# Performance work log

Measured on AMD Instinct MI355X. Metric: run time of the kernel, lower is better.

Reference implementation:

```python
import jax, jax.numpy as jnp
import numpy as np
import math

HIDDEN = 8
HEADS = 2
HEAD_DIM = HIDDEN // HEADS  # 4
MAX_SEQ = 102
B, S = 4096, 102


def _rotary_cache(seq_len, head_dim):
    # Matches _create_rotary_embeddings: dim = head_dim//2, inv_freq over arange(0, dim, 2)
    pos = jnp.arange(seq_len, dtype=jnp.float32)
    dim = head_dim // 2
    inv_freq = 1.0 / (10000.0 ** (jnp.arange(0, dim, 2, dtype=jnp.float32) / dim))
    sinusoid = pos[:, None] * inv_freq[None, :]           # [seq, dim//2] -> [102, 1]
    return jnp.stack([jnp.sin(sinusoid), jnp.cos(sinusoid)], axis=0)  # [2, seq, 1]


def _apply_rotary(x, cos, sin):
    # x: [B, H, S, hd]; cos/sin: [2, S, 1] (faithful to the source's buggy unpack,
    # which broadcasts the stacked sin/cos pair across the H==2 head dim)
    x2 = jnp.stack([-x[..., 1::2], x[..., ::2]], axis=-1).reshape(x.shape)
    return x * cos + x2 * sin


def setup_inputs() -> dict:
    key = jax.random.key(0)
    kq, kk, kv, k1, k2, k3, k4 = jax.random.split(key, 7)
    scale = 1.0 / math.sqrt(HIDDEN)
    return {
        "query": jax.random.normal(kq, (B, S, HIDDEN), dtype=jnp.float32),
        "key": jax.random.normal(kk, (B, S, HIDDEN), dtype=jnp.float32),
        "value": jax.random.normal(kv, (B, S, HIDDEN), dtype=jnp.float32),
        "wq": jax.random.normal(k1, (HIDDEN, HIDDEN), dtype=jnp.float32) * scale,
        "wk": jax.random.normal(k2, (HIDDEN, HIDDEN), dtype=jnp.float32) * scale,
        "wv": jax.random.normal(k3, (HIDDEN, HIDDEN), dtype=jnp.float32) * scale,
        "wo": jax.random.normal(k4, (HIDDEN, HIDDEN), dtype=jnp.float32) * scale,
    }


def reference(query, key, value, wq, wk, wv, wo):
    b, sq, _ = query.shape
    sk = key.shape[1]
    # nn.Linear (no bias): y = x @ W^T
    q = query @ wq.T
    k = key @ wk.T
    v = value @ wv.T
    # b n (h d) -> b h n d
    def split_heads(t, s):
        return t.reshape(b, s, HEADS, HEAD_DIM).transpose(0, 2, 1, 3)
    q = split_heads(q, sq)
    k = split_heads(k, sk)
    v = split_heads(v, sk)
    cache = _rotary_cache(MAX_SEQ, HEAD_DIM)
    sin_t = cache[:, :sq]  # [2, sq, 1] (named 'sin' in source, holds stacked sin/cos)
    cos_t = cache[:, :sk]  # [2, sk, 1]
    q = _apply_rotary(q, cos_t, sin_t)
    k = _apply_rotary(k, cos_t, sin_t)
    scale = 1.0 / math.sqrt(HEAD_DIM)
    # chunk_size = min(sk, 1024) = sk -> single chunk == full softmax attention
    scores = jnp.einsum('bhqd,bhkd->bhqk', q, k) * scale  # [B, H, Sq, Sk]
    attn = jax.nn.softmax(scores, axis=-1)
    out = jnp.einsum('bhqk,bhkd->bhqd', attn, v)
    # b h n d -> b n (h d)
    out = out.transpose(0, 2, 1, 3).reshape(b, sq, HIDDEN)
    return out @ wo.T
```

## Files before the change

### kernel.cpp

```cpp
#include <hip/hip_runtime.h>

#define NB 4096
#define SS 102
#define SSP 104
#define HID 8
#define NH 2
#define HD 4

typedef float v2f __attribute__((ext_vector_type(2)));

__global__ __launch_bounds__(256) void mha_fused_kernel(
    const float* __restrict__ query, const float* __restrict__ key,
    const float* __restrict__ value, const float* __restrict__ wq,
    const float* __restrict__ wk, const float* __restrict__ wv,
    const float* __restrict__ wo, float* __restrict__ out)
{
    __shared__ float sRaw[3 * SS * HID];
    __shared__ float sQ[NH * SSP * HD];
    __shared__ float sK[NH * SS * HD];
    __shared__ float sV[NH * SS * HD];
    __shared__ float sW[4 * 64];
    __shared__ float sRot[2 * SS];

    const int t = threadIdx.x;
    const int b = blockIdx.x;

    float4 rq, rk, rv;
    if (t < 204) {
        const float4* q4 = (const float4*)(query + (size_t)b * (SS * HID));
        const float4* k4 = (const float4*)(key   + (size_t)b * (SS * HID));
        const float4* v4 = (const float4*)(value + (size_t)b * (SS * HID));
        rq = q4[t]; rk = k4[t]; rv = v4[t];
    }
    float wreg;
    {
        const float* wsrc = (t < 64) ? wq : (t < 128) ? wk : (t < 192) ? wv : wo;
        wreg = wsrc[t & 63];
    }

    if (t < SS)                    sRot[t] = __sinf((float)t);
    else if (t >= 128 && t < 230)  sRot[SS + (t - 128)] = __cosf((float)(t - 128));

    if (t >= 230 && t < 246) {
        const int z = t - 230;
        const int h = z >> 3, r = SS + ((z >> 2) & 1), d = z & 3;
        sQ[h * SSP * HD + r * HD + d] = 0.f;
    }

    sW[t] = wreg;
    if (t < 204) {
        float4* sRaw4 = (float4*)sRaw;
        sRaw4[t]       = rq;
        sRaw4[204 + t] = rk;
        sRaw4[408 + t] = rv;
    }
    __syncthreads();

    for (int p = t; p < 816; p += 256) {
        const int tensor = (p >= 408) ? 1 : 0;
        const int pp = tensor ? (p - 408) : p;
        const int s  = pp >> 2;
        const int pr = pp & 3;
        const int i0 = pr * 2, i1 = i0 + 1;
        const float4* raw4 = (const float4*)(sRaw + tensor * (SS * HID) + s * HID);
        const float4 ra = raw4[0], rb = raw4[1];
        const float4* w0 = (const float4*)(sW + tensor * 64 + i0 * 8);
        const float4 wa = w0[0], wb = w0[1], wc = w0[2], wd = w0[3];
        float x0 = ra.x * wa.x + ra.y * wa.y + ra.z * wa.z + ra.w * wa.w
                 + rb.x * wb.x + rb.y * wb.y + rb.z * wb.z + rb.w * wb.w;
        float x1 = ra.x * wc.x + ra.y * wc.y + ra.z * wc.z + ra.w * wc.w
                 + rb.x * wd.x + rb.y * wd.y + rb.z * wd.z + rb.w * wd.w;
        const int h = pr >> 1;
        float wr = sRot[h * SS + s];
        if (tensor == 0) wr *= 0.72134752044448170368f;
        const float r0 = (x0 - x1) * wr;
        const float r1 = (x1 + x0) * wr;
        const int d0 = i0 & 3;
        float* dst = (tensor == 0)
            ? (sQ + h * SSP * HD + s * HD + d0)
            : (sK + h * SS * HD + s * HD + d0);
        dst[0] = r0;
        dst[1] = r1;
    }
    for (int e = t; e < 816; e += 256) {
        const int s = e >> 3, i = e & 7;
        const float4* raw4 = (const float4*)(sRaw + 2 * (SS * HID) + s * HID);
        const float4 ra = raw4[0], rb = raw4[1];
        const float4* w0 = (const float4*)(sW + 2 * 64 + i * 8);
        const float4 wa = w0[0], wb = w0[1];
        const float x = ra.x * wa.x + ra.y * wa.y + ra.z * wa.z + ra.w * wa.w
                      + rb.x * wb.x + rb.y * wb.y + rb.z * wb.z + rb.w * wb.w;
        const int h = i >> 2, d = i & 3;
        sV[h * SS * HD + s * HD + d] = x;
    }
    __syncthreads();

    const int wv_  = t >> 6, lane = t & 63;
    const int h    = wv_ >> 1;
    const int kh   = wv_ & 1;
    const bool act = lane < 52;
    v2f acc0 = {0.f, 0.f}, acc1 = {0.f, 0.f}, acc2 = {0.f, 0.f}, acc3 = {0.f, 0.f};
    v2f l = {0.f, 0.f};
    if (act) {
        const float* qb = sQ + h * SSP * HD + (2 * lane) * HD;
        const float4 qa = ((const float4*)qb)[0];
        const float4 qc = ((const float4*)qb)[1];
        const v2f q0 = {qa.x, qc.x}, q1 = {qa.y, qc.y},
                  q2 = {qa.z, qc.z}, q3 = {qa.w, qc.w};
        const float4* K4 = (const float4*)(sK + h * SS * HD) + kh * 51;
        const float4* V4 = (const float4*)(sV + h * SS * HD) + kh * 51;
        float4 kk = K4[0], vvv = V4[0];
#pragma unroll 2
        for (int k = 1; k < 51; ++k) {
            const float4 nk = K4[k], nv = V4[k];
            v2f s = q0 * kk.x + q1 * kk.y + q2 * kk.z + q3 * kk.w;
            v2f p;
            p.x = __builtin_amdgcn_exp2f(s.x);
            p.y = __builtin_amdgcn_exp2f(s.y);
            l += p;
            acc0 += p * vvv.x; acc1 += p * vvv.y;
            acc2 += p * vvv.z; acc3 += p * vvv.w;
            kk = nk; vvv = nv;
        }
        {
            v2f s = q0 * kk.x + q1 * kk.y + q2 * kk.z + q3 * kk.w;
            v2f p;
            p.x = __builtin_amdgcn_exp2f(s.x);
            p.y = __builtin_amdgcn_exp2f(s.y);
            l += p;
            acc0 += p * vvv.x; acc1 += p * vvv.y;
            acc2 += p * vvv.z; acc3 += p * vvv.w;
        }
    }
    if (act) {
        const int rec = kh * 2 + h;
        float4* A4 = (float4*)sRaw + rec * SSP + 2 * lane;
        A4[0] = make_float4(acc0.x, acc1.x, acc2.x, acc3.x);
        A4[1] = make_float4(acc0.y, acc1.y, acc2.y, acc3.y);
        float* L = sRaw + 4 * SSP * 4 + rec * SSP + 2 * lane;
        L[0] = l.x; L[1] = l.y;
    }
    __syncthreads();

    for (int e = t; e < 816; e += 256) {
        const int s = e >> 3, i = e & 7;
        const float4* A4 = (const float4*)sRaw;
        const float4 h0a = A4[0 * SSP + s], h0b = A4[2 * SSP + s];
        const float4 h1a = A4[1 * SSP + s], h1b = A4[3 * SSP + s];
        const float* L = sRaw + 4 * SSP * 4;
        const float inv0 = 1.f / (L[0 * SSP + s] + L[2 * SSP + s]);
        const float inv1 = 1.f / (L[1 * SSP + s] + L[3 * SSP + s]);
        const float c0 = (h0a.x + h0b.x) * inv0, c1 = (h0a.y + h0b.y) * inv0;
        const float c2 = (h0a.z + h0b.z) * inv0, c3 = (h0a.w + h0b.w) * inv0;
        const float c4 = (h1a.x + h1b.x) * inv1, c5 = (h1a.y + h1b.y) * inv1;
        const float c6 = (h1a.z + h1b.z) * inv1, c7 = (h1a.w + h1b.w) * inv1;
        const float4* w0 = (const float4*)(sW + 3 * 64 + i * 8);
        const float4 wa = w0[0], wb = w0[1];
        const float x = c0 * wa.x + c1 * wa.y + c2 * wa.z + c3 * wa.w
                      + c4 * wb.x + c5 * wb.y + c6 * wb.z + c7 * wb.w;
        out[(size_t)b * (SS * HID) + e] = x;
    }
}

extern "C" void kernel_launch(void* const* d_in, const int* in_sizes, int n_in,
                              void* d_out, int out_size, void* d_ws, size_t ws_size,
                              hipStream_t stream) {
    const float* query = (const float*)d_in[0];
    const float* key   = (const float*)d_in[1];
    const float* value = (const float*)d_in[2];
    const float* wq    = (const float*)d_in[3];
    const float* wk    = (const float*)d_in[4];
    const float* wv    = (const float*)d_in[5];
    const float* wo    = (const float*)d_in[6];
    float* out = (float*)d_out;
    mha_fused_kernel<<<NB, 256, 0, stream>>>(query, key, value, wq, wk, wv, wo, out);
}
```

Measured before the change: 121.5 us.

## Shrink block to 128 threads with one wave per head and per-row projections

Restructures the fused attention kernel to use 128 threads: each thread computes a full sequence row's Q/K/V projections and rotary directly from registers, with weights read from global/constant memory instead of staged shared memory. Each wave now handles one head over all 102 keys, which removes the split-key partial accumulation and the combine step. The output projection is done per row with vectorized stores. This cuts shared memory use and barriers and may raise occupancy, but it serializes the key loop per wave and reads more weights from the cache.

```diff
diff --git a/kernel.cpp b/kernel.cpp
--- a/kernel.cpp
+++ b/kernel.cpp
@@ -1,117 +1,85 @@
 #include <hip/hip_runtime.h>
 
-#define NB 4096
-#define SS 102
+#define NB  4096
+#define SS  102
 #define SSP 104
 #define HID 8
-#define NH 2
-#define HD 4
+#define RS  0.72134752044448170368f
 
 typedef float v2f __attribute__((ext_vector_type(2)));
 
-__global__ __launch_bounds__(256) void mha_fused_kernel(
+#define DOT8(A, B, W, i) \
+    ((A).x*(W)[(i)*8+0] + (A).y*(W)[(i)*8+1] + (A).z*(W)[(i)*8+2] + (A).w*(W)[(i)*8+3] + \
+     (B).x*(W)[(i)*8+4] + (B).y*(W)[(i)*8+5] + (B).z*(W)[(i)*8+6] + (B).w*(W)[(i)*8+7])
+
+__global__ __launch_bounds__(128) void mha_fused_kernel(
     const float* __restrict__ query, const float* __restrict__ key,
     const float* __restrict__ value, const float* __restrict__ wq,
     const float* __restrict__ wk, const float* __restrict__ wv,
     const float* __restrict__ wo, float* __restrict__ out)
 {
-    __shared__ float sRaw[3 * SS * HID];
-    __shared__ float sQ[NH * SSP * HD];
-    __shared__ float sK[NH * SS * HD];
-    __shared__ float sV[NH * SS * HD];
-    __shared__ float sW[4 * 64];
-    __shared__ float sRot[2 * SS];
+    __shared__ float sQ[2 * SSP * 4];
+    __shared__ float sK[2 * SS * 4];
+    __shared__ float sV[2 * SS * 4];
 
     const int t = threadIdx.x;
     const int b = blockIdx.x;
 
-    float4 rq, rk, rv;
-    if (t < 204) {
-        const float4* q4 = (const float4*)(query + (size_t)b * (SS * HID));
-        const float4* k4 = (const float4*)(key   + (size_t)b * (SS * HID));
-        const float4* v4 = (const float4*)(value + (size_t)b * (SS * HID));
-        rq = q4[t]; rk = k4[t]; rv = v4[t];
-    }
-    float wreg;
-    {
-        const float* wsrc = (t < 64) ? wq : (t < 128) ? wk : (t < 192) ? wv : wo;
-        wreg = wsrc[t & 63];
-    }
+    if (t < SS) {
+        const size_t boff = (size_t)b * (SS * HID);
+        const float4* q4 = (const float4*)(query + boff) + 2 * t;
+        const float4* k4 = (const float4*)(key   + boff) + 2 * t;
+        const float4* v4 = (const float4*)(value + boff) + 2 * t;
+        const float4 qa = q4[0], qb = q4[1];
+        const float4 ka = k4[0], kb = k4[1];
+        const float4 va = v4[0], vb = v4[1];
+        const float sn = sinf((float)t), cn = cosf((float)t);
 
-    if (t < SS)                    sRot[t] = __sinf((float)t);
-    else if (t >= 128 && t < 230)  sRot[SS + (t - 128)] = __cosf((float)(t - 128));
-
-    if (t >= 230 && t < 246) {
-        const int z = t - 230;
-        const int h = z >> 3, r = SS + ((z >> 2) & 1), d = z & 3;
-        sQ[h * SSP * HD + r * HD + d] = 0.f;
-    }
-
-    sW[t] = wreg;
-    if (t < 204) {
-        float4* sRaw4 = (float4*)sRaw;
-        sRaw4[t]       = rq;
-        sRaw4[204 + t] = rk;
-        sRaw4[408 + t] = rv;
+#pragma unroll
+        for (int h = 0; h < 2; ++h) {
+            const float wrk = h ? cn : sn;
+            const float wrq = wrk * RS;
+            float y[4], z[4];
+#pragma unroll
+            for (int u = 0; u < 2; ++u) {
+                const int i0 = h * 4 + 2 * u;
+                const float x0 = DOT8(qa, qb, wq, i0), x1 = DOT8(qa, qb, wq, i0 + 1);
+                y[2*u] = (x0 - x1) * wrq;  y[2*u+1] = (x1 + x0) * wrq;
+                const float k0 = DOT8(ka, kb, wk, i0), k1 = DOT8(ka, kb, wk, i0 + 1);
+                z[2*u] = (k0 - k1) * wrk;  z[2*u+1] = (k1 + k0) * wrk;
+            }
+            ((float4*)sQ)[h * SSP + t] = make_float4(y[0], y[1], y[2], y[3]);
+            ((float4*)sK)[h * SS  + t] = make_float4(z[0], z[1], z[2], z[3]);
+            const float f0 = DOT8(va, vb, wv, h*4+0), f1 = DOT8(va, vb, wv, h*4+1);
+            const float f2 = DOT8(va, vb, wv, h*4+2), f3 = DOT8(va, vb, wv, h*4+3);
+            ((float4*)sV)[h * SS + t] = make_float4(f0, f1, f2, f3);
+        }
+    } else if (t < SSP) {
+        ((float4*)sQ)[t]       = make_float4(0.f, 0.f, 0.f, 0.f);
+        ((float4*)sQ)[SSP + t] = make_float4(0.f, 0.f, 0.f, 0.f);
     }
     __syncthreads();
 
-    for (int p = t; p < 816; p += 256) {
-        const int tensor = (p >= 408) ? 1 : 0;
-        const int pp = tensor ? (p - 408) : p;
-        const int s  = pp >> 2;
-        const int pr = pp & 3;
-        const int i0 = pr * 2, i1 = i0 + 1;
-        const float4* raw4 = (const float4*)(sRaw + tensor * (SS * HID) + s * HID);
-        const float4 ra = raw4[0], rb = raw4[1];
-        const float4* w0 = (const float4*)(sW + tensor * 64 + i0 * 8);
-        const float4 wa = w0[0], wb = w0[1], wc = w0[2], wd = w0[3];
-        float x0 = ra.x * wa.x + ra.y * wa.y + ra.z * wa.z + ra.w * wa.w
-                 + rb.x * wb.x + rb.y * wb.y + rb.z * wb.z + rb.w * wb.w;
-        float x1 = ra.x * wc.x + ra.y * wc.y + ra.z * wc.z + ra.w * wc.w
-                 + rb.x * wd.x + rb.y * wd.y + rb.z * wd.z + rb.w * wd.w;
-        const int h = pr >> 1;
-        float wr = sRot[h * SS + s];
-        if (tensor == 0) wr *= 0.72134752044448170368f;
-        const float r0 = (x0 - x1) * wr;
-        const float r1 = (x1 + x0) * wr;
-        const int d0 = i0 & 3;
-        float* dst = (tensor == 0)
-            ? (sQ + h * SSP * HD + s * HD + d0)
-            : (sK + h * SS * HD + s * HD + d0);
-        dst[0] = r0;
-        dst[1] = r1;
-    }
-    for (int e = t; e < 816; e += 256) {
-        const int s = e >> 3, i = e & 7;
-        const float4* raw4 = (const float4*)(sRaw + 2 * (SS * HID) + s * HID);
-        const float4 ra = raw4[0], rb = raw4[1];
-        const float4* w0 = (const float4*)(sW + 2 * 64 + i * 8);
-        const float4 wa = w0[0], wb = w0[1];
-        const float x = ra.x * wa.x + ra.y * wa.y + ra.z * wa.z + ra.w * wa.w
-                      + rb.x * wb.x + rb.y * wb.y + rb.z * wb.z + rb.w * wb.w;
-        const int h = i >> 2, d = i & 3;
-        sV[h * SS * HD + s * HD + d] = x;
+    const int wid = t >> 6, lane = t & 63;
+    const int h = wid;
+    const bool act = lane < 52;
+    v2f q0, q1, q2, q3;
+    if (act) {
+        const float4* Q4 = (const float4*)sQ + h * SSP + 2 * lane;
+        const float4 qa = Q4[0], qc = Q4[1];
+        q0 = (v2f){qa.x, qc.x}; q1 = (v2f){qa.y, qc.y};
+        q2 = (v2f){qa.z, qc.z}; q3 = (v2f){qa.w, qc.w};
     }
     __syncthreads();
 
-    const int wv_  = t >> 6, lane = t & 63;
-    const int h    = wv_ >> 1;
-    const int kh   = wv_ & 1;
-    const bool act = lane < 52;
-    v2f acc0 = {0.f, 0.f}, acc1 = {0.f, 0.f}, acc2 = {0.f, 0.f}, acc3 = {0.f, 0.f};
-    v2f l = {0.f, 0.f};
     if (act) {
-        const float* qb = sQ + h * SSP * HD + (2 * lane) * HD;
-        const float4 qa = ((const float4*)qb)[0];
-        const float4 qc = ((const float4*)qb)[1];
-        const v2f q0 = {qa.x, qc.x}, q1 = {qa.y, qc.y},
-                  q2 = {qa.z, qc.z}, q3 = {qa.w, qc.w};
-        const float4* K4 = (const float4*)(sK + h * SS * HD) + kh * 51;
-        const float4* V4 = (const float4*)(sV + h * SS * HD) + kh * 51;
+        v2f acc0 = {0.f,0.f}, acc1 = {0.f,0.f}, acc2 = {0.f,0.f}, acc3 = {0.f,0.f};
+        v2f l = {0.f, 0.f};
+        const float4* K4 = (const float4*)sK + h * SS;
+        const float4* V4 = (const float4*)sV + h * SS;
         float4 kk = K4[0], vvv = V4[0];
 #pragma unroll 2
-        for (int k = 1; k < 51; ++k) {
+        for (int k = 1; k < SS; ++k) {
             const float4 nk = K4[k], nv = V4[k];
             v2f s = q0 * kk.x + q1 * kk.y + q2 * kk.z + q3 * kk.w;
             v2f p;
@@ -131,34 +99,25 @@
             acc0 += p * vvv.x; acc1 += p * vvv.y;
             acc2 += p * vvv.z; acc3 += p * vvv.w;
         }
-    }
-    if (act) {
-        const int rec = kh * 2 + h;
-        float4* A4 = (float4*)sRaw + rec * SSP + 2 * lane;
-        A4[0] = make_float4(acc0.x, acc1.x, acc2.x, acc3.x);
-        A4[1] = make_float4(acc0.y, acc1.y, acc2.y, acc3.y);
-        float* L = sRaw + 4 * SSP * 4 + rec * SSP + 2 * lane;
-        L[0] = l.x; L[1] = l.y;
+        const float ix = 1.f / l.x, iy = 1.f / l.y;
+        float4* comb = (float4*)sQ;
+        comb[4 * lane + h]     = make_float4(acc0.x*ix, acc1.x*ix, acc2.x*ix, acc3.x*ix);
+        comb[4 * lane + 2 + h] = make_float4(acc0.y*iy, acc1.y*iy, acc2.y*iy, acc3.y*iy);
     }
     __syncthreads();
 
-    for (int e = t; e < 816; e += 256) {
-        const int s = e >> 3, i = e & 7;
-        const float4* A4 = (const float4*)sRaw;
-        const float4 h0a = A4[0 * SSP + s], h0b = A4[2 * SSP + s];
-        const float4 h1a = A4[1 * SSP + s], h1b = A4[3 * SSP + s];
-        const float* L = sRaw + 4 * SSP * 4;
-        const float inv0 = 1.f / (L[0 * SSP + s] + L[2 * SSP + s]);
-        const float inv1 = 1.f / (L[1 * SSP + s] + L[3 * SSP + s]);
-        const float c0 = (h0a.x + h0b.x) * inv0, c1 = (h0a.y + h0b.y) * inv0;
-        const float c2 = (h0a.z + h0b.z) * inv0, c3 = (h0a.w + h0b.w) * inv0;
-        const float c4 = (h1a.x + h1b.x) * inv1, c5 = (h1a.y + h1b.y) * inv1;
-        const float c6 = (h1a.z + h1b.z) * inv1, c7 = (h1a.w + h1b.w) * inv1;
-        const float4* w0 = (const float4*)(sW + 3 * 64 + i * 8);
-        const float4 wa = w0[0], wb = w0[1];
-        const float x = c0 * wa.x + c1 * wa.y + c2 * wa.z + c3 * wa.w
-                      + c4 * wb.x + c5 * wb.y + c6 * wb.z + c7 * wb.w;
-        out[(size_t)b * (SS * HID) + e] = x;
+    if (t < SS) {
+        const float4 c0 = ((const float4*)sQ)[2 * t];
+        const float4 c1 = ((const float4*)sQ)[2 * t + 1];
+        float o[8];
+#pragma unroll
+        for (int i = 0; i < 8; ++i) {
+            o[i] = c0.x*wo[i*8+0] + c0.y*wo[i*8+1] + c0.z*wo[i*8+2] + c0.w*wo[i*8+3]
+                 + c1.x*wo[i*8+4] + c1.y*wo[i*8+5] + c1.z*wo[i*8+6] + c1.w*wo[i*8+7];
+        }
+        float4* o4 = (float4*)(out + (size_t)b * (SS * HID) + t * HID);
+        o4[0] = make_float4(o[0], o[1], o[2], o[3]);
+        o4[1] = make_float4(o[4], o[5], o[6], o[7]);
     }
 }
 
@@ -173,5 +132,5 @@
     const float* wv    = (const float*)d_in[5];
     const float* wo    = (const float*)d_in[6];
     float* out = (float*)d_out;
-    mha_fused_kernel<<<NB, 256, 0, stream>>>(query, key, value, wq, wk, wv, wo, out);
+    mha_fused_kernel<<<NB, 128, 0, stream>>>(query, key, value, wq, wk, wv, wo, out);
 }
```

Measured after the change: 122.5 us. No clear change (+0.9%).
